# Kernel optimization log

Measured on AMD Instinct MI355X. Metric: run time of the kernel, lower is better.

The kernel has to match this reference:

```python
import jax, jax.numpy as jnp
import numpy as np

D_MODEL = 1024
N_HEADS = 16
D_HEAD = D_MODEL // N_HEADS
D_FF = 4 * D_MODEL
EPS = 1e-5


def _layernorm(x, g, b):
    mu = jnp.mean(x, axis=-1, keepdims=True)
    var = jnp.var(x, axis=-1, keepdims=True)
    return (x - mu) * jax.lax.rsqrt(var + EPS) * g + b


def setup_inputs() -> dict:
    key = jax.random.key(0)
    ks = jax.random.split(key, 16)
    s_attn = 1.0 / np.sqrt(D_MODEL)
    s_ff1 = 1.0 / np.sqrt(D_MODEL)
    s_ff2 = 1.0 / np.sqrt(D_FF)
    inp = {
        'x': jax.random.normal(ks[0], (2, 2048, D_MODEL), dtype=jnp.float32),
        'Wq': jax.random.uniform(ks[1], (D_MODEL, D_MODEL), jnp.float32, -s_attn, s_attn),
        'bq': jax.random.uniform(ks[2], (D_MODEL,), jnp.float32, -s_attn, s_attn),
        'Wk': jax.random.uniform(ks[3], (D_MODEL, D_MODEL), jnp.float32, -s_attn, s_attn),
        'bk': jax.random.uniform(ks[4], (D_MODEL,), jnp.float32, -s_attn, s_attn),
        'Wv': jax.random.uniform(ks[5], (D_MODEL, D_MODEL), jnp.float32, -s_attn, s_attn),
        'bv': jax.random.uniform(ks[6], (D_MODEL,), jnp.float32, -s_attn, s_attn),
        'Wo': jax.random.uniform(ks[7], (D_MODEL, D_MODEL), jnp.float32, -s_attn, s_attn),
        'bo': jax.random.uniform(ks[8], (D_MODEL,), jnp.float32, -s_attn, s_attn),
        'W1': jax.random.uniform(ks[9], (D_MODEL, D_FF), jnp.float32, -s_ff1, s_ff1),
        'b1': jax.random.uniform(ks[10], (D_FF,), jnp.float32, -s_ff1, s_ff1),
        'W2': jax.random.uniform(ks[11], (D_FF, D_MODEL), jnp.float32, -s_ff2, s_ff2),
        'b2': jax.random.uniform(ks[12], (D_MODEL,), jnp.float32, -s_ff2, s_ff2),
        'ln1_g': jnp.ones((D_MODEL,), jnp.float32),
        'ln1_b': jnp.zeros((D_MODEL,), jnp.float32),
        'ln2_g': jnp.ones((D_MODEL,), jnp.float32),
        'ln2_b': jnp.zeros((D_MODEL,), jnp.float32),
    }
    return inp


def reference(x, Wq, bq, Wk, bk, Wv, bv, Wo, bo, W1, b1, W2, b2, ln1_g, ln1_b, ln2_g, ln2_b):
    B, T, D = x.shape
    scale = D_HEAD ** -0.5

    # pre-norm MHSA + residual
    h = _layernorm(x, ln1_g, ln1_b)
    def split(z):  # [B,T,D] -> [B,H,T,d_h]
        return z.reshape(B, T, N_HEADS, D_HEAD).transpose(0, 2, 1, 3)
    Q = split(h @ Wq + bq)
    K = split(h @ Wk + bk)
    V = split(h @ Wv + bv)
    scores = jnp.einsum('bhqd,bhkd->bhqk', Q, K) * scale  # [B,H,T,T]
    attn = jax.nn.softmax(scores, axis=-1)
    out = jnp.einsum('bhqk,bhkd->bhqd', attn, V)
    out = out.transpose(0, 2, 1, 3).reshape(B, T, D)
    x = x + (out @ Wo + bo)

    # pre-norm FFN + residual
    h = _layernorm(x, ln2_g, ln2_b)
    ff = jax.nn.gelu(h @ W1 + b1, approximate=False) @ W2 + b2
    return x + ff
```

## Files before the change

### kernel.cpp

```cpp
#include <hip/hip_runtime.h>
#include <math.h>

#define SEQ   2048
#define DM    1024
#define LDQKV 3072
#define MTOK  4096

typedef float  f32x4   __attribute__((ext_vector_type(4)));
typedef __bf16 bf16x8  __attribute__((ext_vector_type(8)));
typedef short  short8  __attribute__((ext_vector_type(8)));
typedef short  short4v __attribute__((ext_vector_type(4)));

__device__ __forceinline__ short f2bf(float f) {
  union { float f; unsigned u; } v; v.f = f;
  unsigned r = v.u + 0x7fffu + ((v.u >> 16) & 1u);
  return (short)(r >> 16);
}

__device__ __forceinline__ void gl_lds16(const void* g, void* l) {
  __builtin_amdgcn_global_load_lds(
      (const __attribute__((address_space(1))) void*)g,
      (__attribute__((address_space(3))) void*)l, 16, 0, 0);
}

__device__ __forceinline__ f32x4 mfma_bf16(bf16x8 a, bf16x8 b, f32x4 c) {
  return __builtin_amdgcn_mfma_f32_16x16x32_bf16(a, b, c, 0, 0, 0);
}

__global__ __launch_bounds__(256) void transpose_cast64_k(
    const float* __restrict__ W, short* __restrict__ Wt, int K, int N)
{
  __shared__ float tile[64][65];
  const int n0 = blockIdx.x * 64, k0 = blockIdx.y * 64;
  const int tid = threadIdx.x;
  const int lr = tid >> 4, lc = (tid & 15) * 4;
#pragma unroll
  for (int i = 0; i < 4; i++) {
    const float4 v = *(const float4*)&W[(size_t)(k0 + lr + i * 16) * N + n0 + lc];
    tile[lr + i * 16][lc]     = v.x;
    tile[lr + i * 16][lc + 1] = v.y;
    tile[lr + i * 16][lc + 2] = v.z;
    tile[lr + i * 16][lc + 3] = v.w;
  }
  __syncthreads();
  const int nr = tid >> 3, ks = (tid & 7) * 8;
#pragma unroll
  for (int i = 0; i < 2; i++) {
    short8 o;
#pragma unroll
    for (int j = 0; j < 8; j++) o[j] = f2bf(tile[ks + j][nr + i * 32]);
    *(short8*)&Wt[(size_t)(n0 + nr + i * 32) * K + k0 + ks] = o;
  }
}

__global__ __launch_bounds__(256) void ln_k(
    const float* __restrict__ x, const float* __restrict__ g,
    const float* __restrict__ b, short* __restrict__ out)
{
  const int row = blockIdx.x;
  const int tid = threadIdx.x;
  const float4 v = ((const float4*)(x + (size_t)row * DM))[tid];
  float s  = v.x + v.y + v.z + v.w;
  float ss = v.x * v.x + v.y * v.y + v.z * v.z + v.w * v.w;
#pragma unroll
  for (int m = 32; m >= 1; m >>= 1) { s += __shfl_xor(s, m); ss += __shfl_xor(ss, m); }
  __shared__ float red[8];
  const int wid = tid >> 6;
  if ((tid & 63) == 0) { red[wid] = s; red[4 + wid] = ss; }
  __syncthreads();
  s  = red[0] + red[1] + red[2] + red[3];
  ss = red[4] + red[5] + red[6] + red[7];
  const float mu  = s * (1.f / DM);
  const float var = ss * (1.f / DM) - mu * mu;
  const float rs  = rsqrtf(var + 1e-5f);
  const float4 gv = ((const float4*)g)[tid];
  const float4 bv = ((const float4*)b)[tid];
  short4v o;
  o[0] = f2bf((v.x - mu) * rs * gv.x + bv.x);
  o[1] = f2bf((v.y - mu) * rs * gv.y + bv.y);
  o[2] = f2bf((v.z - mu) * rs * gv.z + bv.z);
  o[3] = f2bf((v.w - mu) * rs * gv.w + bv.w);
  *(short4v*)(out + (size_t)row * DM + tid * 4) = o;
}

__global__ __launch_bounds__(256) void concat_bias_k(
    const float* __restrict__ bq, const float* __restrict__ bk,
    const float* __restrict__ bv, float* __restrict__ o)
{
  int i = blockIdx.x * 256 + threadIdx.x;
  if (i < 3072) {
    float v = (i < 1024) ? bq[i] : (i < 2048 ? bk[i - 1024] : bv[i - 2048]);
    o[i] = v;
  }
}

__global__ __launch_bounds__(256) void vtrans_k(
    const short* __restrict__ V, short* __restrict__ Vt)
{
  const int b = blockIdx.z, h = blockIdx.y, t0 = blockIdx.x * 64;
  __shared__ short tile[64][72];
  const int tid = threadIdx.x;
  const int r = tid >> 2, c = (tid & 3) * 16;
  const short* src = V + (size_t)(b * SEQ + t0 + r) * LDQKV + h * 64 + c;
  *(short8*)&tile[r][c]     = *(const short8*)src;
  *(short8*)&tile[r][c + 8] = *(const short8*)(src + 8);
  __syncthreads();
  const int d = tid >> 2;
  short8 o0, o1;
#pragma unroll
  for (int k = 0; k < 8; k++) o0[k] = tile[c + k][d];
#pragma unroll
  for (int k = 0; k < 8; k++) o1[k] = tile[c + 8 + k][d];
  short* dst = Vt + (((size_t)(b * 16 + h) * 64) + d) * 2048 + t0 + c;
  *(short8*)dst       = o0;
  *(short8*)(dst + 8) = o1;
}

template <bool GELU_, bool RESID, bool OUTBF16>
__global__ __launch_bounds__(512) void gemm256(
    const short* __restrict__ A, const short* __restrict__ Bt,
    const float* __restrict__ bias, const float* __restrict__ resid,
    void* __restrict__ Cout, int M, int N, int K)
{
  __shared__ __align__(16) short Atile[2][256 * 64];
  __shared__ __align__(16) short Btile[2][256 * 64];

  const int tid = threadIdx.x, lane = tid & 63, wid = tid >> 6;
  const int wm = wid >> 2, wn = wid & 3;

  const int nbn = N >> 8;
  const int chunk = gridDim.x >> 3;
  const int swz = (blockIdx.x & 7) * chunk + (blockIdx.x >> 3);
  const int bm = (swz / nbn) * 256;
  const int bn = (swz % nbn) * 256;

  f32x4 acc[8][4] = {};

  const int srow  = wid * 8 + (lane >> 3);
  const int sslot = (lane & 7) ^ ((lane >> 3) & 7);
  const short* Asrc = A  + (size_t)(bm + srow) * K + sslot * 8;
  const short* Bsrc = Bt + (size_t)(bn + srow) * K + sslot * 8;

#define STAGE256(buf, k0)                                                     \
  {                                                                           \
    _Pragma("unroll")                                                         \
    for (int j = 0; j < 4; j++) {                                             \
      gl_lds16(Asrc + (size_t)(j * 64) * K + (k0), &Atile[buf][(j * 64 + wid * 8) * 64]); \
      gl_lds16(Bsrc + (size_t)(j * 64) * K + (k0), &Btile[buf][(j * 64 + wid * 8) * 64]); \
    }                                                                         \
  }

  const int aRowBase = (wm * 128 + (lane & 15)) * 128;
  const int bRowBase = (wn * 64  + (lane & 15)) * 128;
  const int slot0 = (((lane >> 4)    ) ^ (lane & 7)) * 16;
  const int slot1 = (((lane >> 4) + 4) ^ (lane & 7)) * 16;

#define COMPUTE256(buf)                                                       \
  {                                                                           \
    const char* Ab_ = (const char*)&Atile[buf][0];                            \
    const char* Bb_ = (const char*)&Btile[buf][0];                            \
    _Pragma("unroll")                                                         \
    for (int ks = 0; ks < 2; ks++) {                                          \
      const int sl = ks ? slot1 : slot0;                                      \
      bf16x8 a[8], b[4];                                                      \
      _Pragma("unroll")                                                       \
      for (int mi = 0; mi < 8; mi++)                                          \
        a[mi] = *(const bf16x8*)(Ab_ + aRowBase + mi * 2048 + sl);            \
      _Pragma("unroll")                                                       \
      for (int ni = 0; ni < 4; ni++)                                          \
        b[ni] = *(const bf16x8*)(Bb_ + bRowBase + ni * 2048 + sl);            \
      __builtin_amdgcn_s_setprio(1);                                          \
      _Pragma("unroll")                                                       \
      for (int mi = 0; mi < 8; mi++)                                          \
        _Pragma("unroll")                                                     \
        for (int ni = 0; ni < 4; ni++)                                        \
          acc[mi][ni] = mfma_bf16(a[mi], b[ni], acc[mi][ni]);                 \
      __builtin_amdgcn_s_setprio(0);                                          \
    }                                                                         \
  }

  STAGE256(0, 0);
  __syncthreads();

  int cur = 0;
  const int ntiles = K >> 6;
  for (int t = 1; t < ntiles; ++t) {
    STAGE256(cur ^ 1, t * 64);
    COMPUTE256(cur);
    __syncthreads();
    cur ^= 1;
  }
  COMPUTE256(cur);

#pragma unroll
  for (int mi = 0; mi < 8; mi++) {
#pragma unroll
    for (int ni = 0; ni < 4; ni++) {
      const int col = bn + wn * 64 + ni * 16 + (lane & 15);
      const float bs = bias[col];
#pragma unroll
      for (int j = 0; j < 4; j++) {
        const int row = bm + wm * 128 + mi * 16 + (lane >> 4) * 4 + j;
        float v = acc[mi][ni][j] + bs;
        if (GELU_) v = 0.5f * v * (1.0f + erff(v * 0.70710678118654752f));
        if (RESID) v += resid[(size_t)row * N + col];
        if (OUTBF16) ((short*)Cout)[(size_t)row * N + col] = f2bf(v);
        else         ((float*)Cout)[(size_t)row * N + col] = v;
      }
    }
  }
#undef STAGE256
#undef COMPUTE256
}

template <bool GELU_, bool RESID, bool OUTBF16>
__global__ __launch_bounds__(512) void gemm_bt8(
    const short* __restrict__ A, const short* __restrict__ Bt,
    const float* __restrict__ bias, const float* __restrict__ resid,
    void* __restrict__ Cout, int M, int N, int K)
{
  __shared__ __align__(16) short Ab[2][2][128 * 32];
  __shared__ __align__(16) short Bb[2][2][64 * 32];
  const int tid = threadIdx.x, lane = tid & 63, wid = tid >> 6;
  const int kg = wid >> 2, w2 = wid & 3;
  const int wr = w2 >> 1, wc = w2 & 1;
  const int bm = blockIdx.x * 128, bn = blockIdx.y * 64;

  f32x4 acc[4][2] = {};

  const int r_l = lane >> 2;
  const int c8  = ((lane & 3) ^ ((lane >> 3) & 3)) * 8;
  const short* Ag0 = A  + (size_t)(bm + w2 * 32 + r_l)      * K + c8;
  const short* Ag1 = A  + (size_t)(bm + w2 * 32 + 16 + r_l) * K + c8;
  const short* Bg0 = Bt + (size_t)(bn + w2 * 16 + r_l)      * K + c8;

  const int la0 = (w2 * 32) * 32, la1 = (w2 * 32 + 16) * 32, lb0 = (w2 * 16) * 32;
  const int kbase = kg * 32;
  const int rslot = ((lane >> 4) ^ ((lane >> 1) & 3)) * 8;

  gl_lds16(Ag0 + kbase, &Ab[kg][0][la0]);
  gl_lds16(Ag1 + kbase, &Ab[kg][0][la1]);
  gl_lds16(Bg0 + kbase, &Bb[kg][0][lb0]);
  __syncthreads();

  const int nsteps = K >> 6;
  int cur = 0;
  for (int i = 1; i < nsteps; ++i) {
    const int k0 = i * 64 + kbase;
    const int nxt = cur ^ 1;
    gl_lds16(Ag0 + k0, &Ab[kg][nxt][la0]);
    gl_lds16(Ag1 + k0, &Ab[kg][nxt][la1]);
    gl_lds16(Bg0 + k0, &Bb[kg][nxt][lb0]);

    bf16x8 a[4], b[2];
#pragma unroll
    for (int mi = 0; mi < 4; mi++)
      a[mi] = *(const bf16x8*)&Ab[kg][cur][(wr * 64 + mi * 16 + (lane & 15)) * 32 + rslot];
#pragma unroll
    for (int ni = 0; ni < 2; ni++)
      b[ni] = *(const bf16x8*)&Bb[kg][cur][(wc * 32 + ni * 16 + (lane & 15)) * 32 + rslot];
#pragma unroll
    for (int mi = 0; mi < 4; mi++)
#pragma unroll
      for (int ni = 0; ni < 2; ni++)
        acc[mi][ni] = mfma_bf16(a[mi], b[ni], acc[mi][ni]);

    __syncthreads();
    cur = nxt;
  }

  {
    bf16x8 a[4], b[2];
#pragma unroll
    for (int mi = 0; mi < 4; mi++)
      a[mi] = *(const bf16x8*)&Ab[kg][cur][(wr * 64 + mi * 16 + (lane & 15)) * 32 + rslot];
#pragma unroll
    for (int ni = 0; ni < 2; ni++)
      b[ni] = *(const bf16x8*)&Bb[kg][cur][(wc * 32 + ni * 16 + (lane & 15)) * 32 + rslot];
#pragma unroll
    for (int mi = 0; mi < 4; mi++)
#pragma unroll
      for (int ni = 0; ni < 2; ni++)
        acc[mi][ni] = mfma_bf16(a[mi], b[ni], acc[mi][ni]);
  }

  __syncthreads();

  float* red = (float*)&Ab[0][0][0];
  const int lslot = w2 * 64 + lane;
  if (kg == 1) {
    *(f32x4*)&red[((0 * 256) + lslot) * 4]          = acc[0][0];
    *(f32x4*)&red[((1 * 256) + lslot) * 4]          = acc[0][1];
    *(f32x4*)&red[((2 * 256) + lslot) * 4]          = acc[1][0];
    *(f32x4*)&red[((3 * 256) + lslot) * 4]          = acc[1][1];
  } else {
    *(f32x4*)&red[((1024 + 0 * 256) + lslot) * 4]   = acc[2][0];
    *(f32x4*)&red[((1024 + 1 * 256) + lslot) * 4]   = acc[2][1];
    *(f32x4*)&red[((1024 + 2 * 256) + lslot) * 4]   = acc[3][0];
    *(f32x4*)&red[((1024 + 3 * 256) + lslot) * 4]   = acc[3][1];
  }
  __syncthreads();

#define BT8_STORE(MI, NI)                                                     \
  {                                                                           \
    const int col = bn + wc * 32 + (NI) * 16 + (lane & 15);                   \
    const float bs = bias[col];                                               \
    _Pragma("unroll")                                                         \
    for (int j = 0; j < 4; j++) {                                             \
      const int row = bm + wr * 64 + (MI) * 16 + (lane >> 4) * 4 + j;         \
      float v = acc[MI][NI][j] + bs;                                          \
      if (GELU_) v = 0.5f * v * (1.0f + erff(v * 0.70710678118654752f));      \
      if (RESID) v += resid[(size_t)row * N + col];                           \
      if (OUTBF16) ((short*)Cout)[(size_t)row * N + col] = f2bf(v);           \
      else         ((float*)Cout)[(size_t)row * N + col] = v;                 \
    }                                                                         \
  }

  if (kg == 0) {
    acc[0][0] += *(const f32x4*)&red[((0 * 256) + lslot) * 4];
    acc[0][1] += *(const f32x4*)&red[((1 * 256) + lslot) * 4];
    acc[1][0] += *(const f32x4*)&red[((2 * 256) + lslot) * 4];
    acc[1][1] += *(const f32x4*)&red[((3 * 256) + lslot) * 4];
    BT8_STORE(0, 0); BT8_STORE(0, 1); BT8_STORE(1, 0); BT8_STORE(1, 1);
  } else {
    acc[2][0] += *(const f32x4*)&red[((1024 + 0 * 256) + lslot) * 4];
    acc[2][1] += *(const f32x4*)&red[((1024 + 1 * 256) + lslot) * 4];
    acc[3][0] += *(const f32x4*)&red[((1024 + 2 * 256) + lslot) * 4];
    acc[3][1] += *(const f32x4*)&red[((1024 + 3 * 256) + lslot) * 4];
    BT8_STORE(2, 0); BT8_STORE(2, 1); BT8_STORE(3, 0); BT8_STORE(3, 1);
  }
#undef BT8_STORE
}

__global__ __launch_bounds__(512, 4) void attn_k(
    const short* __restrict__ Qg, const short* __restrict__ Kg,
    const short* __restrict__ Vt, short* __restrict__ Og)
{
  const int phys = blockIdx.x;
  const int lg = (phys & 7) * 64 + (phys >> 3);
  const int q0 = (lg & 15) * 128;
  const int h  = (lg >> 4) & 15;
  const int b  = lg >> 8;

  const int tid = threadIdx.x, lane = tid & 63, w = tid >> 6;
  const int qlane = lane & 15, g = lane >> 4;

  __shared__ __align__(16) short Kl[2][128 * 64];
  __shared__ __align__(16) short Vl[2][64 * 128];

  const size_t qrow = (size_t)(b * SEQ + q0 + w * 16 + qlane) * LDQKV + h * 64;
  const bf16x8 qf0 = *(const bf16x8*)&Qg[qrow + g * 8];
  const bf16x8 qf1 = *(const bf16x8*)&Qg[qrow + 32 + g * 8];

  const int kslot = (lane & 7) ^ ((lane >> 3) & 7);
  const short* Kg_a[2];
#pragma unroll
  for (int i = 0; i < 2; i++) {
    const int r  = i * 64 + w * 8 + (lane >> 3);
    const int kc = r >> 4, gr = (r >> 2) & 3, jr = r & 3;
    const int a  = 32 * (kc & 3) + 8 * gr + 4 * (kc >> 2) + jr;
    Kg_a[i] = Kg + ((size_t)(b * SEQ) + a) * LDQKV + h * 64 + kslot * 8;
  }
  const short* Vg_s[2];
#pragma unroll
  for (int i = 0; i < 2; i++) {
    const int d  = i * 32 + w * 4 + (lane >> 4);
    const int vs = (lane & 15) ^ (d & 15);
    Vg_s[i] = Vt + ((size_t)(b * 16 + h) * 64 + d) * 2048 + vs * 8;
  }

  float m_run = -1e30f, l_run = 0.f;
  f32x4 oacc[4] = {};
  const float C = 0.125f * 1.44269504088896f;

#pragma unroll
  for (int i = 0; i < 2; i++) {
    gl_lds16(Kg_a[i], &Kl[0][(i * 64 + w * 8) * 64]);
    gl_lds16(Vg_s[i], &Vl[0][(i * 32 + w * 4) * 128]);
  }
  __syncthreads();

  int cur = 0;
  for (int kt = 0; kt < SEQ; kt += 128) {
    const int nxt = cur ^ 1;
    if (kt + 128 < SEQ) {
#pragma unroll
      for (int i = 0; i < 2; i++) {
        gl_lds16(Kg_a[i] + (size_t)(kt + 128) * LDQKV, &Kl[nxt][(i * 64 + w * 8) * 64]);
        gl_lds16(Vg_s[i] + (kt + 128),                 &Vl[nxt][(i * 32 + w * 4) * 128]);
      }
    }
    const char* KbC = (const char*)&Kl[cur][0];
    const char* VbC = (const char*)&Vl[cur][0];

    f32x4 s[8];
#pragma unroll
    for (int kc = 0; kc < 8; kc++) {
      const int kr = kc * 16 + qlane;
      const char* kp = KbC + kr * 128;
      const int sw = (kr & 7) << 4;
      bf16x8 kf0 = *(const bf16x8*)(kp + ((g * 16) ^ sw));
      bf16x8 kf1 = *(const bf16x8*)(kp + ((64 + g * 16) ^ sw));
      f32x4 z = {};
      z = mfma_bf16(kf0, qf0, z);
      z = mfma_bf16(kf1, qf1, z);
      s[kc] = z;
    }

    f32x4 m4 = s[0];
#pragma unroll
    for (int kc = 1; kc < 8; kc++) {
      m4[0] = fmaxf(m4[0], s[kc][0]); m4[1] = fmaxf(m4[1], s[kc][1]);
      m4[2] = fmaxf(m4[2], s[kc][2]); m4[3] = fmaxf(m4[3], s[kc][3]);
    }
    float mt = fmaxf(fmaxf(m4[0], m4[1]), fmaxf(m4[2], m4[3]));
    mt = fmaxf(mt, __shfl_xor(mt, 16));
    mt = fmaxf(mt, __shfl_xor(mt, 32));

    if (!__all(mt - m_run <= 40.0f)) {
      const float mnew = fmaxf(m_run, mt);
      const float r = __builtin_amdgcn_exp2f((m_run - mnew) * C);
      m_run = mnew;
      l_run *= r;
#pragma unroll
      for (int j = 0; j < 4; j++) {
        const float rj = __shfl(r, g * 4 + j);
#pragma unroll
        for (int dt = 0; dt < 4; dt++) oacc[dt][j] *= rj;
      }
    }

    const float nmc = -m_run * C;
    float rs = 0.f;
    unsigned pw[4][4];
#pragma unroll
    for (int kc = 0; kc < 8; kc++) {
      f32x4 p;
#pragma unroll
      for (int j = 0; j < 4; j++) p[j] = __builtin_amdgcn_exp2f(fmaf(s[kc][j], C, nmc));
      rs += (p[0] + p[1]) + (p[2] + p[3]);
      unsigned w0, w1;
      asm("v_cvt_pk_bf16_f32 %0, %1, %2" : "=v"(w0) : "v"(p[0]), "v"(p[1]));
      asm("v_cvt_pk_bf16_f32 %0, %1, %2" : "=v"(w1) : "v"(p[2]), "v"(p[3]));
      pw[kc & 3][2 * (kc >> 2) + 0] = w0;
      pw[kc & 3][2 * (kc >> 2) + 1] = w1;
    }
    rs += __shfl_xor(rs, 16);
    rs += __shfl_xor(rs, 32);
    l_run += rs;

#pragma unroll
    for (int ks = 0; ks < 4; ks++) {
      union { unsigned u[4]; bf16x8 v; } pf;
      pf.u[0] = pw[ks][0]; pf.u[1] = pw[ks][1];
      pf.u[2] = pw[ks][2]; pf.u[3] = pw[ks][3];
#pragma unroll
      for (int dt = 0; dt < 4; dt++) {
        const int vr = dt * 16 + qlane;
        bf16x8 vf = *(const bf16x8*)(VbC + vr * 256 + ((64 * ks + 16 * g) ^ ((vr & 15) << 4)));
        oacc[dt] = mfma_bf16(pf.v, vf, oacc[dt]);
      }
    }

    __syncthreads();
    cur = nxt;
  }

  const float linv = 1.f / l_run;
#pragma unroll
  for (int j = 0; j < 4; j++) {
    const float lj = __shfl(linv, g * 4 + j);
    const int tok = q0 + w * 16 + g * 4 + j;
#pragma unroll
    for (int dt = 0; dt < 4; dt++)
      Og[(size_t)(b * SEQ + tok) * DM + h * 64 + dt * 16 + qlane] = f2bf(oacc[dt][j] * lj);
  }
}

extern "C" void kernel_launch(void* const* d_in, const int* in_sizes, int n_in,
                              void* d_out, int out_size, void* d_ws, size_t ws_size,
                              hipStream_t stream)
{
  const float* x    = (const float*)d_in[0];
  const float* Wq   = (const float*)d_in[1];
  const float* bq   = (const float*)d_in[2];
  const float* Wk   = (const float*)d_in[3];
  const float* bk   = (const float*)d_in[4];
  const float* Wv   = (const float*)d_in[5];
  const float* bv   = (const float*)d_in[6];
  const float* Wo   = (const float*)d_in[7];
  const float* bo   = (const float*)d_in[8];
  const float* W1   = (const float*)d_in[9];
  const float* b1   = (const float*)d_in[10];
  const float* W2   = (const float*)d_in[11];
  const float* b2   = (const float*)d_in[12];
  const float* ln1g = (const float*)d_in[13];
  const float* ln1b = (const float*)d_in[14];
  const float* ln2g = (const float*)d_in[15];
  const float* ln2b = (const float*)d_in[16];

  char* ws = (char*)d_ws;
  const size_t MB = 1024 * 1024;
  short* Wqkvt = (short*)(ws + 0 * MB);
  short* Wqt   = Wqkvt;
  short* Wkt   = (short*)(ws + 2 * MB);
  short* Wvt   = (short*)(ws + 4 * MB);
  short* Wot   = (short*)(ws + 6 * MB);
  short* W1t   = (short*)(ws + 8 * MB);
  short* W2t   = (short*)(ws + 16 * MB);
  short* hbuf  = (short*)(ws + 24 * MB);
  short* QKV   = (short*)(ws + 32 * MB);
  short* AO    = (short*)(ws + 56 * MB);
  float* x1    = (float*)(ws + 64 * MB);
  short* Vtb   = (short*)(ws + 64 * MB);
  float* bqkv  = (float*)(ws + 80 * MB);
  short* gbuf  = (short*)(ws + 32 * MB);

  dim3 tb(256);

  transpose_cast64_k<<<dim3(16, 16), tb, 0, stream>>>(Wq, Wqt, 1024, 1024);
  transpose_cast64_k<<<dim3(16, 16), tb, 0, stream>>>(Wk, Wkt, 1024, 1024);
  transpose_cast64_k<<<dim3(16, 16), tb, 0, stream>>>(Wv, Wvt, 1024, 1024);
  transpose_cast64_k<<<dim3(16, 16), tb, 0, stream>>>(Wo, Wot, 1024, 1024);
  transpose_cast64_k<<<dim3(64, 16), tb, 0, stream>>>(W1, W1t, 1024, 4096);
  transpose_cast64_k<<<dim3(16, 64), tb, 0, stream>>>(W2, W2t, 4096, 1024);
  concat_bias_k<<<dim3(12), tb, 0, stream>>>(bq, bk, bv, bqkv);

  ln_k<<<dim3(MTOK), tb, 0, stream>>>(x, ln1g, ln1b, hbuf);

  gemm256<false, false, true><<<dim3(192), dim3(512), 0, stream>>>(
      hbuf, Wqkvt, bqkv, nullptr, QKV, MTOK, 3072, 1024);

  vtrans_k<<<dim3(32, 16, 2), tb, 0, stream>>>(QKV + 2048, Vtb);

  attn_k<<<dim3(512), dim3(512), 0, stream>>>(QKV, QKV + 1024, Vtb, AO);

  gemm_bt8<false, true, false><<<dim3(32, 16), dim3(512), 0, stream>>>(
      AO, Wot, bo, x, x1, MTOK, 1024, 1024);

  ln_k<<<dim3(MTOK), tb, 0, stream>>>(x1, ln2g, ln2b, hbuf);

  gemm256<true, false, true><<<dim3(256), dim3(512), 0, stream>>>(
      hbuf, W1t, b1, nullptr, gbuf, MTOK, 4096, 1024);

  gemm_bt8<false, true, false><<<dim3(32, 16), dim3(512), 0, stream>>>(
      gbuf, W2t, b2, x1, (float*)d_out, MTOK, 1024, 4096);
}
```

Before: 256.9 us.

## Add 4-stage pipelined FFN1 GEMM, polynomial GELU, and merged weight transpose

Adds a new GEMM variant for the W1 projection that uses a 4-buffer LDS ring with BK=32, explicit vmcnt waits, raised MFMA priority, and an XCD-aware block swizzle, so global loads overlap compute more deeply. It replaces erff in the GELU epilogue with an Abramowitz-Stegun polynomial built from hardware rcp and exp2, which cuts epilogue cost but slightly changes accuracy. It also merges the six weight transpose-cast launches into one kernel to reduce launch overhead.

```diff
diff --git a/kernel.cpp b/kernel.cpp
--- a/kernel.cpp
+++ b/kernel.cpp
@@ -27,11 +27,45 @@
   return __builtin_amdgcn_mfma_f32_16x16x32_bf16(a, b, c, 0, 0, 0);
 }
 
-__global__ __launch_bounds__(256) void transpose_cast64_k(
-    const float* __restrict__ W, short* __restrict__ Wt, int K, int N)
-{
+__device__ __forceinline__ float gelu_f(float x) {
+  const float z  = x * 0.70710678118654752f;
+  const float az = fabsf(z);
+  const float t  = __builtin_amdgcn_rcpf(fmaf(0.3275911f, az, 1.0f));
+  float p = fmaf(1.061405429f, t, -1.453152027f);
+  p = fmaf(p, t, 1.421413741f);
+  p = fmaf(p, t, -0.284496736f);
+  p = fmaf(p, t, 0.254829592f);
+  p = p * t;
+  const float e = __builtin_amdgcn_exp2f(az * az * -1.4426950408889634f);
+  float erfp = fmaf(-p, e, 1.0f);
+  erfp = (z < 0.f) ? -erfp : erfp;
+  return x * fmaf(0.5f, erfp, 0.5f);
+}
+
+__global__ __launch_bounds__(256) void transpose_all_k(
+    const float* __restrict__ Wq, const float* __restrict__ Wk,
+    const float* __restrict__ Wv, const float* __restrict__ Wo,
+    const float* __restrict__ W1, const float* __restrict__ W2,
+    short* __restrict__ Wqt, short* __restrict__ Wkt, short* __restrict__ Wvt,
+    short* __restrict__ Wot, short* __restrict__ W1t, short* __restrict__ W2t)
+{
+  const int bid = blockIdx.x;
+  const float* W; short* Wt; int K, N, nx, ky;
+  if (bid < 1024) {
+    const int m = bid >> 8, r = bid & 255;
+    W  = (m == 0) ? Wq : (m == 1) ? Wk : (m == 2) ? Wv : Wo;
+    Wt = (m == 0) ? Wqt : (m == 1) ? Wkt : (m == 2) ? Wvt : Wot;
+    K = 1024; N = 1024; nx = r & 15; ky = r >> 4;
+  } else if (bid < 2048) {
+    const int r = bid - 1024;
+    W = W1; Wt = W1t; K = 1024; N = 4096; nx = r & 63; ky = r >> 6;
+  } else {
+    const int r = bid - 2048;
+    W = W2; Wt = W2t; K = 4096; N = 1024; nx = r & 15; ky = r >> 4;
+  }
+  const int n0 = nx * 64, k0 = ky * 64;
+
   __shared__ float tile[64][65];
-  const int n0 = blockIdx.x * 64, k0 = blockIdx.y * 64;
   const int tid = threadIdx.x;
   const int lr = tid >> 4, lc = (tid & 15) * 4;
 #pragma unroll
@@ -202,7 +236,7 @@
       for (int j = 0; j < 4; j++) {
         const int row = bm + wm * 128 + mi * 16 + (lane >> 4) * 4 + j;
         float v = acc[mi][ni][j] + bs;
-        if (GELU_) v = 0.5f * v * (1.0f + erff(v * 0.70710678118654752f));
+        if (GELU_) v = gelu_f(v);
         if (RESID) v += resid[(size_t)row * N + col];
         if (OUTBF16) ((short*)Cout)[(size_t)row * N + col] = f2bf(v);
         else         ((float*)Cout)[(size_t)row * N + col] = v;
@@ -211,6 +245,104 @@
   }
 #undef STAGE256
 #undef COMPUTE256
+}
+
+template <bool GELU_, bool RESID, bool OUTBF16>
+__global__ __launch_bounds__(512) void gemm256d3(
+    const short* __restrict__ A, const short* __restrict__ Bt,
+    const float* __restrict__ bias, const float* __restrict__ resid,
+    void* __restrict__ Cout, int M, int N, int K)
+{
+  __shared__ __align__(16) short Ash[4][256 * 32];
+  __shared__ __align__(16) short Bsh[4][256 * 32];
+
+  const int tid = threadIdx.x, lane = tid & 63, wid = tid >> 6;
+  const int wm = wid >> 2, wn = wid & 3;
+
+  const int nbn = N >> 8;
+  const int chunk = gridDim.x >> 3;
+  const int swz = (blockIdx.x & 7) * chunk + (blockIdx.x >> 3);
+  const int bm = (swz / nbn) * 256;
+  const int bn = (swz % nbn) * 256;
+
+  f32x4 acc[8][4] = {};
+
+  const int srow = tid >> 2;
+  const int scol = ((tid & 3) ^ ((srow >> 1) & 3)) * 8;
+  const short* Asrc = A  + (size_t)(bm + srow) * K + scol;
+  const short* Bsrc = Bt + (size_t)(bn + srow) * K + scol;
+  const int d0 = (wid * 16) * 32, d1 = (128 + wid * 16) * 32;
+
+#define STAGE_D3(buf, k0)                                                     \
+  {                                                                           \
+    gl_lds16(Asrc + (k0),                   &Ash[buf][d0]);                   \
+    gl_lds16(Asrc + (size_t)128 * K + (k0), &Ash[buf][d1]);                   \
+    gl_lds16(Bsrc + (k0),                   &Bsh[buf][d0]);                   \
+    gl_lds16(Bsrc + (size_t)128 * K + (k0), &Bsh[buf][d1]);                   \
+  }
+
+  const int rslot = ((lane >> 4) ^ ((lane >> 1) & 3)) * 8;
+  const int aOff  = (wm * 128 + (lane & 15)) * 32 + rslot;
+  const int bOff  = (wn * 64  + (lane & 15)) * 32 + rslot;
+
+#define COMPUTE_D3(buf)                                                       \
+  {                                                                           \
+    const short* Ab_ = &Ash[buf][0];                                          \
+    const short* Bb_ = &Bsh[buf][0];                                          \
+    bf16x8 a[8], b[4];                                                        \
+    _Pragma("unroll")                                                         \
+    for (int mi = 0; mi < 8; mi++)                                            \
+      a[mi] = *(const bf16x8*)(Ab_ + aOff + mi * 512);                        \
+    _Pragma("unroll")                                                         \
+    for (int ni = 0; ni < 4; ni++)                                            \
+      b[ni] = *(const bf16x8*)(Bb_ + bOff + ni * 512);                        \
+    __builtin_amdgcn_s_setprio(1);                                            \
+    _Pragma("unroll")                                                         \
+    for (int mi = 0; mi < 8; mi++)                                            \
+      _Pragma("unroll")                                                       \
+      for (int ni = 0; ni < 4; ni++)                                          \
+        acc[mi][ni] = mfma_bf16(a[mi], b[ni], acc[mi][ni]);                   \
+    __builtin_amdgcn_s_setprio(0);                                            \
+  }
+
+  const int nt = K >> 5;
+
+  STAGE_D3(0, 0);
+  STAGE_D3(1, 32);
+  STAGE_D3(2, 64);
+  asm volatile("s_waitcnt vmcnt(8)" ::: "memory");
+  __builtin_amdgcn_s_barrier();
+  __builtin_amdgcn_sched_barrier(0);
+
+  for (int t = 0; t < nt; ++t) {
+    if (t + 3 < nt) STAGE_D3((t + 3) & 3, (t + 3) * 32);
+    COMPUTE_D3(t & 3);
+    if (t + 3 < nt)      { asm volatile("s_waitcnt vmcnt(8)" ::: "memory"); }
+    else if (t + 2 < nt) { asm volatile("s_waitcnt vmcnt(4)" ::: "memory"); }
+    else if (t + 1 < nt) { asm volatile("s_waitcnt vmcnt(0)" ::: "memory"); }
+    __builtin_amdgcn_s_barrier();
+    __builtin_amdgcn_sched_barrier(0);
+  }
+
+#pragma unroll
+  for (int mi = 0; mi < 8; mi++) {
+#pragma unroll
+    for (int ni = 0; ni < 4; ni++) {
+      const int col = bn + wn * 64 + ni * 16 + (lane & 15);
+      const float bs = bias[col];
+#pragma unroll
+      for (int j = 0; j < 4; j++) {
+        const int row = bm + wm * 128 + mi * 16 + (lane >> 4) * 4 + j;
+        float v = acc[mi][ni][j] + bs;
+        if (GELU_) v = gelu_f(v);
+        if (RESID) v += resid[(size_t)row * N + col];
+        if (OUTBF16) ((short*)Cout)[(size_t)row * N + col] = f2bf(v);
+        else         ((float*)Cout)[(size_t)row * N + col] = v;
+      }
+    }
+  }
+#undef STAGE_D3
+#undef COMPUTE_D3
 }
 
 template <bool GELU_, bool RESID, bool OUTBF16>
@@ -289,15 +421,15 @@
   float* red = (float*)&Ab[0][0][0];
   const int lslot = w2 * 64 + lane;
   if (kg == 1) {
-    *(f32x4*)&red[((0 * 256) + lslot) * 4]          = acc[0][0];
-    *(f32x4*)&red[((1 * 256) + lslot) * 4]          = acc[0][1];
-    *(f32x4*)&red[((2 * 256) + lslot) * 4]          = acc[1][0];
-    *(f32x4*)&red[((3 * 256) + lslot) * 4]          = acc[1][1];
+    *(f32x4*)&red[((0 * 256) + lslot) * 4]        = acc[0][0];
+    *(f32x4*)&red[((1 * 256) + lslot) * 4]        = acc[0][1];
+    *(f32x4*)&red[((2 * 256) + lslot) * 4]        = acc[1][0];
+    *(f32x4*)&red[((3 * 256) + lslot) * 4]        = acc[1][1];
   } else {
-    *(f32x4*)&red[((1024 + 0 * 256) + lslot) * 4]   = acc[2][0];
-    *(f32x4*)&red[((1024 + 1 * 256) + lslot) * 4]   = acc[2][1];
-    *(f32x4*)&red[((1024 + 2 * 256) + lslot) * 4]   = acc[3][0];
-    *(f32x4*)&red[((1024 + 3 * 256) + lslot) * 4]   = acc[3][1];
+    *(f32x4*)&red[((1024 + 0 * 256) + lslot) * 4] = acc[2][0];
+    *(f32x4*)&red[((1024 + 1 * 256) + lslot) * 4] = acc[2][1];
+    *(f32x4*)&red[((1024 + 2 * 256) + lslot) * 4] = acc[3][0];
+    *(f32x4*)&red[((1024 + 3 * 256) + lslot) * 4] = acc[3][1];
   }
   __syncthreads();
 
@@ -309,7 +441,7 @@
     for (int j = 0; j < 4; j++) {                                             \
       const int row = bm + wr * 64 + (MI) * 16 + (lane >> 4) * 4 + j;         \
       float v = acc[MI][NI][j] + bs;                                          \
-      if (GELU_) v = 0.5f * v * (1.0f + erff(v * 0.70710678118654752f));      \
+      if (GELU_) v = gelu_f(v);                                               \
       if (RESID) v += resid[(size_t)row * N + col];                           \
       if (OUTBF16) ((short*)Cout)[(size_t)row * N + col] = f2bf(v);           \
       else         ((float*)Cout)[(size_t)row * N + col] = v;                 \
@@ -518,12 +650,8 @@
 
   dim3 tb(256);
 
-  transpose_cast64_k<<<dim3(16, 16), tb, 0, stream>>>(Wq, Wqt, 1024, 1024);
-  transpose_cast64_k<<<dim3(16, 16), tb, 0, stream>>>(Wk, Wkt, 1024, 1024);
-  transpose_cast64_k<<<dim3(16, 16), tb, 0, stream>>>(Wv, Wvt, 1024, 1024);
-  transpose_cast64_k<<<dim3(16, 16), tb, 0, stream>>>(Wo, Wot, 1024, 1024);
-  transpose_cast64_k<<<dim3(64, 16), tb, 0, stream>>>(W1, W1t, 1024, 4096);
-  transpose_cast64_k<<<dim3(16, 64), tb, 0, stream>>>(W2, W2t, 4096, 1024);
+  transpose_all_k<<<dim3(3072), tb, 0, stream>>>(
+      Wq, Wk, Wv, Wo, W1, W2, Wqt, Wkt, Wvt, Wot, W1t, W2t);
   concat_bias_k<<<dim3(12), tb, 0, stream>>>(bq, bk, bv, bqkv);
 
   ln_k<<<dim3(MTOK), tb, 0, stream>>>(x, ln1g, ln1b, hbuf);
@@ -540,7 +668,7 @@
 
   ln_k<<<dim3(MTOK), tb, 0, stream>>>(x1, ln2g, ln2b, hbuf);
 
-  gemm256<true, false, true><<<dim3(256), dim3(512), 0, stream>>>(
+  gemm256d3<true, false, true><<<dim3(256), dim3(512), 0, stream>>>(
       hbuf, W1t, b1, nullptr, gbuf, MTOK, 4096, 1024);
 
   gemm_bt8<false, true, false><<<dim3(32, 16), dim3(512), 0, stream>>>(
```

Result: faster. 243.8 us (-5.1%).
